# Optimization experiments

Measured on AMD Instinct MI355X. Metric: run time of the kernel, lower is better.

Reference implementation:

```python
import jax, jax.numpy as jnp
import numpy as np

B, S, L, K, E, V = 2048, 4, 16, 8, 256, 128  # batch, max_steps, tokens/step, landmarks/cell, emb_sz, vocab


def setup_inputs() -> dict:
    key = jax.random.key(0)
    ks = jax.random.split(key, 10)
    std = 1.0 / (E * 9)
    return {
        "gold_table": jax.random.normal(ks[0], (11, E), jnp.float32),
        "map_table": jax.random.normal(ks[1], (V, E), jnp.float32) * 0.01,  # init_std=0.01
        "conv_weight": jax.random.uniform(ks[2], (E, E, 3, 3), jnp.float32, -std, std),
        "action_table": jax.random.normal(ks[3], (4, 32), jnp.float32),
        "action_W": jax.random.normal(ks[4], (9, 32), jnp.float32) * (1.0 / np.sqrt(32.0)),
        "action_b": jnp.zeros((9,), jnp.float32),
        "goldstandard": jax.random.randint(ks[5], (B, S, L), 0, 11),
        "actions": jax.random.randint(ks[6], (B, S - 1), 0, 4),
        "landmarks": jax.random.randint(ks[7], (B, 4, 4, K), 0, V),
        "y": jax.random.randint(ks[8], (B, 2), 0, 4),
    }


def _extract_patches(x):
    # x: [B,E,4,4] -> [B,9,E,16]; 3x3 neighborhoods with zero padding (conv padding=1)
    xp = jnp.pad(x, ((0, 0), (0, 0), (1, 1), (1, 1)))
    shifts = [xp[:, :, dh:dh + 4, dw:dw + 4].reshape(x.shape[0], x.shape[1], 16)
              for dh in range(3) for dw in range(3)]
    return jnp.stack(shifts, axis=1)


def reference(gold_table, map_table, conv_weight, action_table, action_W, action_b,
              goldstandard, actions, landmarks, y):
    Bn = y.shape[0]
    # goldstandard features: per-step embed+sum over tokens, concat over steps -> [B, S*E]
    emb = gold_table[goldstandard].sum(axis=2).reshape(Bn, -1)
    # MapEmbedding2d with padding_idx=0: zero row 0, embed, sum over landmark list
    mt = map_table.at[0].set(0.0)
    l_emb = mt[landmarks].sum(axis=3).transpose(0, 3, 1, 2)  # [B,E,4,4]
    # action-conditioned 3x3 masks, one per action
    action_out = action_table @ action_W.T + action_b  # [4,9]
    masks = jax.nn.softmax(action_out, axis=1)  # [4,9]
    Wr = conv_weight.reshape(E, E, 9)  # [O,I,tap]
    l_embs = [l_emb]
    cur = l_emb
    for j in range(S - 1):
        # per-sample routed mask == dispatch-to-expert conv; fused gather+masked-conv+scatter
        m = masks[actions[:, j]]  # [B,9]
        patches = _extract_patches(cur)  # [B,9,E,16]
        out = jnp.einsum('btip,bt,oit->bop', patches, m, Wr).reshape(Bn, E, 4, 4)
        l_embs.append(out)
        cur = out
    lm = jnp.concatenate(l_embs, axis=1).reshape(Bn, S * E, 16)  # [B, S*E, 16]
    logits = jnp.einsum('bcp,bc->bp', lm, emb)  # bmm(landmarks^T, emb)
    prob = jax.nn.softmax(logits, axis=1)
    y_true = y[:, 0] * 4 + y[:, 1]
    # torch CrossEntropyLoss applied to prob (softmax twice, as in the original)
    logp = jax.nn.log_softmax(prob, axis=1)
    loss = -jnp.take_along_axis(logp, y_true[:, None], axis=1).mean()
    acc = (jnp.argmax(prob, axis=1) == y_true).astype(jnp.float32).mean()
    return loss, acc, prob
```

## Files before the change

kernel.cpp:

```cpp
#include <hip/hip_runtime.h>
#include <hip/hip_bf16.h>

typedef __attribute__((ext_vector_type(4))) float f32x4;
typedef __attribute__((ext_vector_type(8))) short short8;

__device__ __forceinline__ float bf2f(ushort u) {
    union { unsigned int u; float f; } x; x.u = ((unsigned int)u) << 16; return x.f;
}
__device__ __forceinline__ ushort f2bf(float f) {
    union { float f; unsigned int u; } x; x.f = f;
    unsigned int u = x.u;
    unsigned int r = (u + 0x7fffu + ((u >> 16) & 1u)) >> 16;
    return (ushort)r;
}
__device__ __forceinline__ void gload16(const ushort* g, ushort* l) {
    __builtin_amdgcn_global_load_lds(
        (const __attribute__((address_space(1))) unsigned int*)g,
        (__attribute__((address_space(3))) unsigned int*)l, 16, 0, 0);
}

__global__ __launch_bounds__(256) void k_front(
    const float* __restrict__ conv_w, const float* __restrict__ a_table,
    const float* __restrict__ a_W, const float* __restrict__ a_b,
    const int* __restrict__ actions, const float* __restrict__ mapt,
    const int* __restrict__ lms, int* __restrict__ cnt,
    int* __restrict__ list, ushort* __restrict__ Wa,
    ushort* __restrict__ c0, float* __restrict__ out_head)
{
    const int bid = blockIdx.x, tid = threadIdx.x;

    {
        const int e4 = (tid & 63) * 4, pw = tid >> 6;
        #pragma unroll
        for (int pp = 0; pp < 4; ++pp) {
            const int p = pw * 4 + pp;
            const int* lm = lms + (bid * 16 + p) * 8;
            float4 s = make_float4(0.f, 0.f, 0.f, 0.f);
            #pragma unroll
            for (int k = 0; k < 8; ++k) {
                const int idx = lm[k];
                if (idx) {
                    const float4 v = *(const float4*)&mapt[idx * 256 + e4];
                    s.x += v.x; s.y += v.y; s.z += v.z; s.w += v.w;
                }
            }
            ushort o4[4] = { f2bf(s.x), f2bf(s.y), f2bf(s.z), f2bf(s.w) };
            *(uint2*)&c0[(size_t)(bid * 16 + p) * 256 + e4] = *(const uint2*)o4;
        }
    }

    if (bid < 256) {
        __shared__ float ao[4][9];
        __shared__ float m[4][9];
        if (tid < 36) {
            const int a = tid / 9, t = tid % 9;
            float s = a_b[t];
            for (int c = 0; c < 32; c++) s += a_table[a * 32 + c] * a_W[t * 32 + c];
            ao[a][t] = s;
        }
        __syncthreads();
        if (tid < 4) {
            float mx = -1e30f;
            for (int t = 0; t < 9; t++) mx = fmaxf(mx, ao[tid][t]);
            float e[9], z = 0.f;
            for (int t = 0; t < 9; t++) { e[t] = expf(ao[tid][t] - mx); z += e[t]; }
            for (int t = 0; t < 9; t++) m[tid][t] = e[t] / z;
        }
        __syncthreads();
        const int o = bid;
        float w9[9];
        #pragma unroll
        for (int t = 0; t < 9; t++) w9[t] = conv_w[(o * 256 + tid) * 9 + t];
        #pragma unroll
        for (int a = 0; a < 4; a++)
            #pragma unroll
            for (int t = 0; t < 9; t++)
                Wa[(size_t)((a << 8) + o) * 2304 + t * 256 + tid] = f2bf(m[a][t] * w9[t]);
    } else if (bid == 256) {
        if (tid < 12) cnt[tid] = 0;
        if (tid == 0) { out_head[0] = 0.f; out_head[1] = 0.f; }
        __syncthreads();
        for (int it = 0; it < 24; it++) {
            const int idx = it * 256 + tid;
            const int jj = idx >> 11, b = idx & 2047;
            const int av = actions[b * 3 + jj];
            const int pos = atomicAdd(&cnt[jj * 4 + av], 1);
            list[((jj * 4 + av) << 11) + pos] = b;
        }
    }
}

__global__ __launch_bounds__(256, 2) void k_conv(
    const ushort* __restrict__ cur, const ushort* __restrict__ Wa,
    const int* __restrict__ cnt, const int* __restrict__ list,
    const int j, ushort* __restrict__ outp)
{
    __shared__ __align__(16) ushort Alds[2][128 * 64];
    __shared__ __align__(16) ushort Blds[4 * 17 * 256];
    const int tid = threadIdx.x, bid = blockIdx.x;
    const int a = bid & 3, om = (bid >> 2) & 1, grp = bid >> 3;
    const int ca = cnt[j * 4 + a];
    if (grp * 4 >= ca) return;
    const int* la = list + ((j * 4 + a) << 11) + grp * 4;

    const int wid = tid >> 6, lane = tid & 63;
    const int l15 = lane & 15, l4 = lane >> 4;
    const int wm = wid >> 1, wn = wid & 1;

    {
        const int sw = (grp * 4 + wid < ca) ? la[wid] : la[0];
        const ushort* src = cur + (size_t)sw * 4096;
        const int p = lane >> 2, cg = lane & 3;
        ushort* dst = Blds + wid * 4352 + p * 256;
        #pragma unroll
        for (int qq = 0; qq < 8; ++qq) {
            const int c = qq * 4 + cg;
            const uint4 v = *(const uint4*)(src + p * 256 + c * 8);
            *(uint4*)(dst + (c ^ (p & 7)) * 8) = v;
        }
        if (lane < 32) {
            const short8 z = {0, 0, 0, 0, 0, 0, 0, 0};
            *(short8*)(Blds + wid * 4352 + 16 * 256 + lane * 8) = z;
        }
    }

    int sid[2]; bool vst[2];
    #pragma unroll
    for (int nf = 0; nf < 2; ++nf) {
        const int sl = wn * 2 + nf;
        vst[nf] = (grp * 4 + sl) < ca;
        sid[nf] = vst[nf] ? la[sl] : 0;
    }

    const ushort* wbase = Wa + (size_t)((a << 8) + om * 128) * 2304;
    const int srow = tid >> 3, sc = tid & 7;
    #define STAGE(buf, k0)                                                     \
        _Pragma("unroll")                                                      \
        for (int qq = 0; qq < 4; ++qq) {                                       \
            const int row = qq * 32 + srow;                                    \
            const int cc = sc ^ (row & 7);                                     \
            gload16(wbase + (size_t)row * 2304 + (k0) + cc * 8,                \
                    &Alds[buf][qq * 2048 + tid * 8]);                          \
        }

    f32x4 acc[4][2];
    #pragma unroll
    for (int mf = 0; mf < 4; ++mf) {
        acc[mf][0] = (f32x4){0.f, 0.f, 0.f, 0.f};
        acc[mf][1] = (f32x4){0.f, 0.f, 0.f, 0.f};
    }

    const int ph = l15 >> 2, pw = l15 & 3;
    const ushort* b0base = Blds + (wn * 2 + 0) * 4352;
    const ushort* b1base = Blds + (wn * 2 + 1) * 4352;

    STAGE(0, 0);
    __syncthreads();

    int cb = 0;
    for (int ks = 0; ks < 36; ++ks) {
        if (ks + 1 < 36) STAGE(cb ^ 1, (ks + 1) * 64);
        const int t = ks >> 2;
        const int td = (t * 11) >> 5, tm = t - td * 3;
        const int hh = ph + td - 1, ww = pw + tm - 1;
        const bool xv = (hh >= 0) & (hh < 4) & (ww >= 0) & (ww < 4);
        const int brow = xv ? ((hh << 2) + ww) : 16;
        const int rbase = brow * 256, rx = brow & 7;
        const int ch0 = (ks & 3) * 8;

        #pragma unroll
        for (int kf = 0; kf < 2; ++kf) {
            const int bch = ((ch0 + kf * 4 + l4) ^ rx) * 8;
            const short8 bf0 = *(const short8*)(b0base + rbase + bch);
            const short8 bf1 = *(const short8*)(b1base + rbase + bch);
            #pragma unroll
            for (int mf = 0; mf < 4; ++mf) {
                const int rr = wm * 64 + mf * 16 + l15;
                const int acx = ((kf * 4 + l4) ^ (rr & 7)) * 8;
                const short8 af = *(const short8*)&Alds[cb][rr * 64 + acx];
                acc[mf][0] = __builtin_amdgcn_mfma_f32_16x16x32_bf16(
                    af, bf0, acc[mf][0], 0, 0, 0);
                acc[mf][1] = __builtin_amdgcn_mfma_f32_16x16x32_bf16(
                    af, bf1, acc[mf][1], 0, 0, 0);
            }
        }
        __syncthreads();
        cb ^= 1;
    }

    #pragma unroll
    for (int nf = 0; nf < 2; ++nf) {
        if (!vst[nf]) continue;
        const size_t rowb = ((size_t)sid[nf] * 16 + l15) * 256;
        #pragma unroll
        for (int mf = 0; mf < 4; ++mf) {
            const int ob = om * 128 + wm * 64 + mf * 16 + l4 * 4;
            ushort o4[4];
            #pragma unroll
            for (int r = 0; r < 4; r++) o4[r] = f2bf(acc[mf][nf][r]);
            *(uint2*)&outp[rowb + ob] = *(const uint2*)o4;
        }
    }
    #undef STAGE
}

__global__ __launch_bounds__(256) void k_final(
    const ushort* __restrict__ c0, const ushort* __restrict__ c1,
    const ushort* __restrict__ c2, const ushort* __restrict__ c3,
    const float* __restrict__ gold, const int* __restrict__ gs,
    const int* __restrict__ y, float* __restrict__ d_out)
{
    __shared__ float embl[4][272];
    __shared__ float lg[16];
    const int b = blockIdx.x, tid = threadIdx.x;
    {
        const int s = tid >> 6, e0 = (tid & 63) * 4;
        const int* g = gs + b * 64 + s * 16;
        float4 accv = make_float4(0.f, 0.f, 0.f, 0.f);
        #pragma unroll
        for (int l = 0; l < 16; l++) {
            const float4 v = *(const float4*)&gold[g[l] * 256 + e0];
            accv.x += v.x; accv.y += v.y; accv.z += v.z; accv.w += v.w;
        }
        float* dst = &embl[s][(e0 >> 4) * 17 + (e0 & 15)];
        dst[0] = accv.x; dst[1] = accv.y; dst[2] = accv.z; dst[3] = accv.w;
    }
    __syncthreads();
    const int p = tid >> 4, g16 = tid & 15;
    const ushort* rows[4] = {
        c0 + (size_t)(b * 16 + p) * 256, c1 + (size_t)(b * 16 + p) * 256,
        c2 + (size_t)(b * 16 + p) * 256, c3 + (size_t)(b * 16 + p) * 256 };
    float acc = 0.f;
    #pragma unroll
    for (int s = 0; s < 4; s++) {
        const ushort* row = rows[s] + g16 * 16;
        const uint4 v0 = *(const uint4*)row;
        const uint4 v1 = *(const uint4*)(row + 8);
        const ushort* pv0 = (const ushort*)&v0;
        const ushort* pv1 = (const ushort*)&v1;
        const float* eb = &embl[s][g16 * 17];
        #pragma unroll
        for (int q = 0; q < 8; q++) acc += bf2f(pv0[q]) * eb[q];
        #pragma unroll
        for (int q = 0; q < 8; q++) acc += bf2f(pv1[q]) * eb[8 + q];
    }
    acc += __shfl_xor(acc, 1);
    acc += __shfl_xor(acc, 2);
    acc += __shfl_xor(acc, 4);
    acc += __shfl_xor(acc, 8);
    if (g16 == 0) lg[p] = acc;
    __syncthreads();
    if (tid == 0) {
        float mx = -1e30f;
        for (int q = 0; q < 16; q++) mx = fmaxf(mx, lg[q]);
        float ex[16], z = 0.f;
        for (int q = 0; q < 16; q++) { ex[q] = expf(lg[q] - mx); z += ex[q]; }
        float prob[16];
        for (int q = 0; q < 16; q++) {
            prob[q] = ex[q] / z;
            d_out[2 + b * 16 + q] = prob[q];
        }
        int am = 0; float bv = prob[0];
        for (int q = 1; q < 16; q++) if (prob[q] > bv) { bv = prob[q]; am = q; }
        const int yt = y[b * 2] * 4 + y[b * 2 + 1];
        float z2 = 0.f;
        for (int q = 0; q < 16; q++) z2 += expf(prob[q]);
        const float logp = prob[yt] - logf(z2);
        atomicAdd(&d_out[0], -logp * (1.0f / 2048.0f));
        atomicAdd(&d_out[1], (am == yt) ? (1.0f / 2048.0f) : 0.0f);
    }
}

extern "C" void kernel_launch(void* const* d_in, const int* in_sizes, int n_in,
                              void* d_out, int out_size, void* d_ws, size_t ws_size,
                              hipStream_t stream) {
    const float* gold_table = (const float*)d_in[0];
    const float* map_table  = (const float*)d_in[1];
    const float* conv_w     = (const float*)d_in[2];
    const float* a_table    = (const float*)d_in[3];
    const float* a_W        = (const float*)d_in[4];
    const float* a_b        = (const float*)d_in[5];
    const int*   gs         = (const int*)d_in[6];
    const int*   actions    = (const int*)d_in[7];
    const int*   lms        = (const int*)d_in[8];
    const int*   y          = (const int*)d_in[9];
    float* out = (float*)d_out;

    char* ws = (char*)d_ws;
    int*    cnt  = (int*)(ws + 0);
    int*    list = (int*)(ws + 256);
    ushort* Wa   = (ushort*)(ws + 131072);
    ushort* c0   = (ushort*)(ws + 4849664);
    ushort* c1   = (ushort*)(ws + 21626880);
    ushort* c2   = (ushort*)(ws + 38404096);
    ushort* c3   = (ushort*)(ws + 55181312);
    (void)in_sizes; (void)n_in; (void)out_size; (void)ws_size;

    k_front<<<2048, 256, 0, stream>>>(conv_w, a_table, a_W, a_b, actions,
                                      map_table, lms, cnt, list, Wa, c0, out);
    k_conv <<<4096, 256, 0, stream>>>(c0, Wa, cnt, list, 0, c1);
    k_conv <<<4096, 256, 0, stream>>>(c1, Wa, cnt, list, 1, c2);
    k_conv <<<4096, 256, 0, stream>>>(c2, Wa, cnt, list, 2, c3);
    k_final<<<2048, 256, 0, stream>>>(c0, c1, c2, c3, gold_table, gs, y, out);
}
```

Before: 423.3 us.

## Widen conv blocks to 8 samples with triple-buffered weight staging

Each conv block now has 512 threads (8 waves) and covers 8 samples instead of 4, so each staged 128x64 weight tile in LDS is reused across twice as many samples. The weight ring grows from double to triple buffering. Synchronisation is now a manual vmcnt wait plus s_barrier, so loads for two steps ahead stay in flight while the current step computes. The zero padding row in LDS is dropped and out-of-bounds taps are zeroed in registers instead; the cost is more LDS per block and one block per SM.

Result: slower. 455.7 us (+7.7%).

```diff
diff --git a/kernel.cpp b/kernel.cpp
--- a/kernel.cpp
+++ b/kernel.cpp
@@ -90,37 +90,34 @@
     }
 }
 
-__global__ __launch_bounds__(256, 2) void k_conv(
+__global__ __launch_bounds__(512, 1) void k_conv(
     const ushort* __restrict__ cur, const ushort* __restrict__ Wa,
     const int* __restrict__ cnt, const int* __restrict__ list,
     const int j, ushort* __restrict__ outp)
 {
-    __shared__ __align__(16) ushort Alds[2][128 * 64];
-    __shared__ __align__(16) ushort Blds[4 * 17 * 256];
+    __shared__ __align__(16) ushort Alds[3][128 * 64];
+    __shared__ __align__(16) ushort Blds[8 * 16 * 256];
     const int tid = threadIdx.x, bid = blockIdx.x;
     const int a = bid & 3, om = (bid >> 2) & 1, grp = bid >> 3;
     const int ca = cnt[j * 4 + a];
-    if (grp * 4 >= ca) return;
-    const int* la = list + ((j * 4 + a) << 11) + grp * 4;
+    if (grp * 8 >= ca) return;
+    const int* la = list + ((j * 4 + a) << 11) + grp * 8;
 
     const int wid = tid >> 6, lane = tid & 63;
     const int l15 = lane & 15, l4 = lane >> 4;
-    const int wm = wid >> 1, wn = wid & 1;
+    const int wm = wid >> 2, wn = wid & 3;
 
     {
-        const int sw = (grp * 4 + wid < ca) ? la[wid] : la[0];
+        const int sw = (grp * 8 + wid < ca) ? la[wid] : la[0];
         const ushort* src = cur + (size_t)sw * 4096;
         const int p = lane >> 2, cg = lane & 3;
-        ushort* dst = Blds + wid * 4352 + p * 256;
+        ushort* dst = Blds + wid * 4096 + p * 256;
+        const ushort* s2 = src + p * 256;
         #pragma unroll
         for (int qq = 0; qq < 8; ++qq) {
             const int c = qq * 4 + cg;
-            const uint4 v = *(const uint4*)(src + p * 256 + c * 8);
-            *(uint4*)(dst + (c ^ (p & 7)) * 8) = v;
-        }
-        if (lane < 32) {
-            const short8 z = {0, 0, 0, 0, 0, 0, 0, 0};
-            *(short8*)(Blds + wid * 4352 + 16 * 256 + lane * 8) = z;
+            const uint4 v = *(const uint4*)(s2 + c * 8);
+            *(uint4*)(dst + ((c ^ (p & 7)) * 8)) = v;
         }
     }
 
@@ -128,19 +125,19 @@
     #pragma unroll
     for (int nf = 0; nf < 2; ++nf) {
         const int sl = wn * 2 + nf;
-        vst[nf] = (grp * 4 + sl) < ca;
+        vst[nf] = (grp * 8 + sl) < ca;
         sid[nf] = vst[nf] ? la[sl] : 0;
     }
 
     const ushort* wbase = Wa + (size_t)((a << 8) + om * 128) * 2304;
-    const int srow = tid >> 3, sc = tid & 7;
     #define STAGE(buf, k0)                                                     \
         _Pragma("unroll")                                                      \
-        for (int qq = 0; qq < 4; ++qq) {                                       \
-            const int row = qq * 32 + srow;                                    \
-            const int cc = sc ^ (row & 7);                                     \
+        for (int qq = 0; qq < 2; ++qq) {                                       \
+            const int u = qq * 512 + tid;                                      \
+            const int row = u >> 3;                                            \
+            const int cc = (u & 7) ^ (row & 7);                                \
             gload16(wbase + (size_t)row * 2304 + (k0) + cc * 8,                \
-                    &Alds[buf][qq * 2048 + tid * 8]);                          \
+                    &Alds[buf][u * 8]);                                        \
         }
 
     f32x4 acc[4][2];
@@ -151,42 +148,62 @@
     }
 
     const int ph = l15 >> 2, pw = l15 & 3;
-    const ushort* b0base = Blds + (wn * 2 + 0) * 4352;
-    const ushort* b1base = Blds + (wn * 2 + 1) * 4352;
+    const short8 bzero = {0, 0, 0, 0, 0, 0, 0, 0};
+    const ushort* bbase0 = Blds + (wn * 2 + 0) * 4096;
+    const ushort* bbase1 = Blds + (wn * 2 + 1) * 4096;
+    const int asw = l15 & 7;
+
+    #define COMPUTE(ks, rd)                                                    \
+        {                                                                      \
+            const int t = (ks) >> 2;                                           \
+            const int td = (t * 11) >> 5, tm = t - td * 3;                     \
+            const int hh = ph + td - 1, ww = pw + tm - 1;                      \
+            const bool xv = (hh >= 0) & (hh < 4) & (ww >= 0) & (ww < 4);       \
+            const int brow = xv ? ((hh << 2) + ww) : 0;                        \
+            const int rb = brow * 256, rx = brow & 7;                          \
+            _Pragma("unroll")                                                  \
+            for (int kf = 0; kf < 2; ++kf) {                                   \
+                const int bch = ((((ks) & 3) * 8 + kf * 4 + l4) ^ rx) * 8;     \
+                short8 b0 = *(const short8*)(bbase0 + rb + bch);               \
+                short8 b1 = *(const short8*)(bbase1 + rb + bch);               \
+                if (!xv) { b0 = bzero; b1 = bzero; }                           \
+                const int acx = ((kf * 4 + l4) ^ asw) * 8;                     \
+                _Pragma("unroll")                                              \
+                for (int mf = 0; mf < 4; ++mf) {                               \
+                    const int rr = wm * 64 + mf * 16 + l15;                    \
+                    const short8 af =                                          \
+                        *(const short8*)&Alds[rd][rr * 64 + acx];              \
+                    acc[mf][0] = __builtin_amdgcn_mfma_f32_16x16x32_bf16(      \
+                        af, b0, acc[mf][0], 0, 0, 0);                          \
+                    acc[mf][1] = __builtin_amdgcn_mfma_f32_16x16x32_bf16(      \
+                        af, b1, acc[mf][1], 0, 0, 0);                          \
+                }                                                              \
+            }                                                                  \
+        }
 
     STAGE(0, 0);
-    __syncthreads();
-
-    int cb = 0;
-    for (int ks = 0; ks < 36; ++ks) {
-        if (ks + 1 < 36) STAGE(cb ^ 1, (ks + 1) * 64);
-        const int t = ks >> 2;
-        const int td = (t * 11) >> 5, tm = t - td * 3;
-        const int hh = ph + td - 1, ww = pw + tm - 1;
-        const bool xv = (hh >= 0) & (hh < 4) & (ww >= 0) & (ww < 4);
-        const int brow = xv ? ((hh << 2) + ww) : 16;
-        const int rbase = brow * 256, rx = brow & 7;
-        const int ch0 = (ks & 3) * 8;
-
-        #pragma unroll
-        for (int kf = 0; kf < 2; ++kf) {
-            const int bch = ((ch0 + kf * 4 + l4) ^ rx) * 8;
-            const short8 bf0 = *(const short8*)(b0base + rbase + bch);
-            const short8 bf1 = *(const short8*)(b1base + rbase + bch);
-            #pragma unroll
-            for (int mf = 0; mf < 4; ++mf) {
-                const int rr = wm * 64 + mf * 16 + l15;
-                const int acx = ((kf * 4 + l4) ^ (rr & 7)) * 8;
-                const short8 af = *(const short8*)&Alds[cb][rr * 64 + acx];
-                acc[mf][0] = __builtin_amdgcn_mfma_f32_16x16x32_bf16(
-                    af, bf0, acc[mf][0], 0, 0, 0);
-                acc[mf][1] = __builtin_amdgcn_mfma_f32_16x16x32_bf16(
-                    af, bf1, acc[mf][1], 0, 0, 0);
-            }
-        }
-        __syncthreads();
-        cb ^= 1;
-    }
+    STAGE(1, 64);
+    asm volatile("s_waitcnt lgkmcnt(0)" ::: "memory");
+
+    int rd = 0, st = 2;
+    for (int ks = 0; ks < 34; ++ks) {
+        asm volatile("s_waitcnt vmcnt(2)" ::: "memory");
+        __builtin_amdgcn_s_barrier();
+        __builtin_amdgcn_sched_barrier(0);
+        STAGE(st, (ks + 2) * 64);
+        COMPUTE(ks, rd);
+        rd = (rd == 2) ? 0 : rd + 1;
+        st = (st == 2) ? 0 : st + 1;
+    }
+    asm volatile("s_waitcnt vmcnt(2)" ::: "memory");
+    __builtin_amdgcn_s_barrier();
+    __builtin_amdgcn_sched_barrier(0);
+    COMPUTE(34, rd);
+    rd = (rd == 2) ? 0 : rd + 1;
+    asm volatile("s_waitcnt vmcnt(0)" ::: "memory");
+    __builtin_amdgcn_s_barrier();
+    __builtin_amdgcn_sched_barrier(0);
+    COMPUTE(35, rd);
 
     #pragma unroll
     for (int nf = 0; nf < 2; ++nf) {
@@ -202,6 +219,7 @@
         }
     }
     #undef STAGE
+    #undef COMPUTE
 }
 
 __global__ __launch_bounds__(256) void k_final(
@@ -298,8 +316,8 @@
 
     k_front<<<2048, 256, 0, stream>>>(conv_w, a_table, a_W, a_b, actions,
                                       map_table, lms, cnt, list, Wa, c0, out);
-    k_conv <<<4096, 256, 0, stream>>>(c0, Wa, cnt, list, 0, c1);
-    k_conv <<<4096, 256, 0, stream>>>(c1, Wa, cnt, list, 1, c2);
-    k_conv <<<4096, 256, 0, stream>>>(c2, Wa, cnt, list, 2, c3);
+    k_conv <<<2048, 512, 0, stream>>>(c0, Wa, cnt, list, 0, c1);
+    k_conv <<<2048, 512, 0, stream>>>(c1, Wa, cnt, list, 1, c2);
+    k_conv <<<2048, 512, 0, stream>>>(c2, Wa, cnt, list, 2, c3);
     k_final<<<2048, 256, 0, stream>>>(c0, c1, c2, c3, gold_table, gs, y, out);
 }
```
